# Performance work log

Hardware: AMD Instinct MI355X
Metric: run time of the kernel (lower is better)

## Reference

```python
import jax, jax.numpy as jnp
import numpy as np

WH, WW = 12, 12
NUM_HEADS = 8
NW = 4


def _relative_position_index():
    ch, cw = np.meshgrid(np.arange(WH), np.arange(WW), indexing='ij')
    coords = np.stack([ch, cw]).reshape(2, -1)            # [2, Wh*Ww]
    rel = coords[:, :, None] - coords[:, None, :]         # [2, M, M]
    rel = rel.transpose(1, 2, 0)                          # [M, M, 2]
    rel[:, :, 0] += WH - 1
    rel[:, :, 1] += WW - 1
    rel[:, :, 0] *= 2 * WW - 1
    return jnp.asarray(rel.sum(-1))                       # [M, M] int


def setup_inputs() -> dict:
    key = jax.random.key(0)
    ks = jax.random.split(key, 11)
    C = 512
    B_, N = 512, WH * WW + 1
    std = 0.02
    return {
        'x': jax.random.normal(ks[0], (B_, N, C), dtype=jnp.float32),
        'mask': jnp.zeros((NW, N, N), dtype=jnp.float32),
        'rpb_table': jax.random.normal(ks[1], ((2 * WH - 1) * (2 * WW - 1), NUM_HEADS), dtype=jnp.float32) * std,
        'Wq': jax.random.normal(ks[2], (C, C), dtype=jnp.float32) * (C ** -0.5),
        'bq': jax.random.normal(ks[3], (C,), dtype=jnp.float32) * std,
        'Wk': jax.random.normal(ks[4], (C, C), dtype=jnp.float32) * (C ** -0.5),
        'bk': jax.random.normal(ks[5], (C,), dtype=jnp.float32) * std,
        'Wv': jax.random.normal(ks[6], (C, C), dtype=jnp.float32) * (C ** -0.5),
        'bv': jax.random.normal(ks[7], (C,), dtype=jnp.float32) * std,
        'Wo': jax.random.normal(ks[8], (C, C), dtype=jnp.float32) * (C ** -0.5),
        'bo': jax.random.normal(ks[9], (C,), dtype=jnp.float32) * std,
    }


def reference(x, mask, rpb_table, Wq, bq, Wk, bk, Wv, bv, Wo, bo):
    B_, N, C = x.shape
    H = NUM_HEADS
    hd = C // H
    scale = hd ** -0.5
    B = B_ // NW
    M = WH * WW  # window tokens (N = M + 1 global token)

    def proj(W, b):
        return (x @ W.T + b).reshape(B_, N, H, hd).transpose(0, 2, 1, 3)  # [B_,H,N,hd]

    q = proj(Wq, bq)
    k = proj(Wk, bk)
    v = proj(Wv, bv)

    attn = jnp.einsum('bhnd,bhmd->bhnm', q, k) * scale  # [B_,H,N,N]

    rel_idx = _relative_position_index()                 # [M,M]
    bias = rpb_table[rel_idx].transpose(2, 0, 1)          # [H,M,M]
    attn = attn.at[:, :, :M, :M].add(bias[None])          # N != M: bias on window block only

    # shifted-window mask: (nW, N, N)
    attn = (attn.reshape(B, NW, H, N, N) + mask[None, :, None]).reshape(B_, H, N, N)

    # ---- global-token attention redistribution (gx) ----
    ga = attn[:, :, -1, :].reshape(B, NW, H, N).transpose(0, 2, 1, 3)   # [B,H,NW,N]
    g1 = ga[:, :, :, :M].reshape(B, H, NW * M)                           # window keys, all windows
    g2 = ga[:, :, :, M].mean(-1, keepdims=True)                          # mean global-global logit [B,H,1]
    g = jax.nn.softmax(jnp.concatenate([g1, g2], axis=-1), axis=-1)      # [B,H,NW*M+1]
    g1 = g[:, :, :-1].reshape(B, H, NW, M).transpose(0, 2, 1, 3).reshape(B_, H, M)
    g2 = jnp.broadcast_to(g[:, :, -1][:, None, :], (B, NW, H)).reshape(B_, H, 1)
    ga_full = jnp.concatenate([g1, g2], axis=-1)[:, :, None, :]          # [B_,H,1,N]
    gx = jnp.einsum('bhqn,bhnd->bhqd', ga_full, v).transpose(0, 2, 1, 3).reshape(B_, C)
    gx = gx.reshape(B, NW, C).sum(1)                                     # sum over windows [B,C]
    gx = jnp.broadcast_to(gx[:, None, :], (B, NW, C)).reshape(B_, C)

    # ---- standard window attention ----
    attn = jax.nn.softmax(attn, axis=-1)
    out = jnp.einsum('bhnm,bhmd->bhnd', attn, v).transpose(0, 2, 1, 3).reshape(B_, N, C)
    out = out.at[:, -1, :].set(gx)
    return out @ Wo.T + bo
```

## Files before the change

### kernel.cpp

```cpp
#include <hip/hip_runtime.h>
#include <hip/hip_bf16.h>
#include <stdint.h>

#define NTOK 145
#define MTOK 144
#define CDIM 512
#define NHEAD 8
#define HD 64
#define NWIN 4
#define BWIN 512
#define MROWS (BWIN*NTOK)

typedef short short8 __attribute__((ext_vector_type(8)));
typedef float f32x4 __attribute__((ext_vector_type(4)));

__device__ __forceinline__ uint16_t f2bf(float f) {
  union { float f; uint32_t u; } x; x.f = f;
  uint32_t r = x.u + 0x7FFFu + ((x.u >> 16) & 1u);
  return (uint16_t)(r >> 16);
}
__device__ __forceinline__ float bf2f(uint16_t u) {
  union { uint32_t u; float f; } x; x.u = ((uint32_t)u) << 16; return x.f;
}
__device__ __forceinline__ uint32_t pack2(float a, float b) {
  return (uint32_t)f2bf(a) | ((uint32_t)f2bf(b) << 16);
}

#define GLL(gp, lp) __builtin_amdgcn_global_load_lds( \
    (const __attribute__((address_space(1))) uint32_t*)(gp), \
    (__attribute__((address_space(3))) uint32_t*)(lp), 16, 0, 0)

__global__ __launch_bounds__(256) void cast_x(const float* __restrict__ x,
                                              uint16_t* __restrict__ xb) {
  size_t id = ((size_t)blockIdx.x*256 + threadIdx.x)*8;
  float4 a = *(const float4*)(x+id), c = *(const float4*)(x+id+4);
  uint4 o = make_uint4(pack2(a.x,a.y), pack2(a.z,a.w), pack2(c.x,c.y), pack2(c.z,c.w));
  *(uint4*)(xb+id) = o;
}

__global__ void prep_kernel(const float* __restrict__ rpb,
                            const float* __restrict__ Wq, const float* __restrict__ bq,
                            const float* __restrict__ Wk, const float* __restrict__ bk,
                            const float* __restrict__ Wv, const float* __restrict__ bv,
                            const float* __restrict__ Wo,
                            uint16_t* __restrict__ wqkv, uint16_t* __restrict__ wo,
                            float* __restrict__ bqkv, float* __restrict__ biastab) {
  int id = blockIdx.x * 256 + threadIdx.x;
  const int A = 1536*512, B = 512*512, C2 = 1536, D = 8*144*144;
  if (id < A) {
    int n = id >> 9, k = id & 511;
    const float* W = (n < 512) ? Wq : (n < 1024) ? Wk : Wv;
    wqkv[id] = f2bf(W[(size_t)(n & 511)*512 + k]);
  } else if ((id -= A) < B) {
    wo[id] = f2bf(Wo[id]);
  } else if ((id -= B) < C2) {
    bqkv[id] = (id < 512) ? bq[id] : (id < 1024) ? bk[id-512] : bv[id-1024];
  } else if ((id -= C2) < D) {
    int h = id / (144*144); int rr = id % (144*144);
    int i = rr / 144, j = rr % 144;
    int rel = (i/12 - j/12 + 11) * 23 + (i%12 - j%12 + 11);
    biastab[id] = rpb[rel*8 + h];
  }
}

__global__ __launch_bounds__(256) void gemm_qkv(
    const uint16_t* __restrict__ xb, const uint16_t* __restrict__ wqkv,
    const float* __restrict__ bqkv,
    uint16_t* __restrict__ qb, uint16_t* __restrict__ kb, uint16_t* __restrict__ vb) {
  __shared__ __align__(16) uint16_t As[128*32];
  __shared__ __align__(16) uint16_t Bs[128*32];
  int bid = blockIdx.x;
  int mb, nb;
  if (bid < 6912) { int g = bid / 96, r = bid % 96; mb = g*8 + (r & 7); nb = r >> 3; }
  else           { int r = bid - 6912;              mb = 576 + (r & 3); nb = r >> 2; }
  int tid = threadIdx.x;
  int lane = tid & 63, w = tid >> 6;
  int wm = w >> 1, wn = w & 1;
  int lm = lane & 15, lq = lane >> 4;

  int srow = lane >> 2, scol = (lane & 3) * 8;
  const uint16_t* agp = xb   + (size_t)(mb*128 + w*32 + srow)*512 + scol;
  const uint16_t* bgp = wqkv + (size_t)(nb*128 + w*32 + srow)*512 + scol;
  uint16_t* Asw = &As[w*32*32];
  uint16_t* Bsw = &Bs[w*32*32];

  f32x4 acc[4][4];
#pragma unroll
  for (int a = 0; a < 4; a++)
#pragma unroll
    for (int b = 0; b < 4; b++) acc[a][b] = (f32x4){0.f,0.f,0.f,0.f};

  for (int kt = 0; kt < 16; kt++) {
    GLL(agp + kt*32,          Asw);
    GLL(agp + kt*32 + 16*512, Asw + 16*32);
    GLL(bgp + kt*32,          Bsw);
    GLL(bgp + kt*32 + 16*512, Bsw + 16*32);
    __syncthreads();
    short8 a[4], b[4];
#pragma unroll
    for (int t = 0; t < 4; t++) a[t] = *(short8*)&As[(wm*64 + t*16 + lm)*32 + lq*8];
#pragma unroll
    for (int t = 0; t < 4; t++) b[t] = *(short8*)&Bs[(wn*64 + t*16 + lm)*32 + lq*8];
#pragma unroll
    for (int tm = 0; tm < 4; tm++)
#pragma unroll
      for (int tn = 0; tn < 4; tn++)
        acc[tm][tn] = __builtin_amdgcn_mfma_f32_16x16x32_bf16(a[tm], b[tn], acc[tm][tn], 0, 0, 0);
    __syncthreads();
  }
#pragma unroll
  for (int tn = 0; tn < 4; tn++) {
    int n = nb*128 + wn*64 + tn*16 + lm;
    float bias = bqkv[n];
    int which = n >> 9, c = n & 511;
    uint16_t* dst = (which == 0) ? qb : (which == 1) ? kb : vb;
    int hh = c >> 6, dd = c & 63;
#pragma unroll
    for (int tm = 0; tm < 4; tm++) {
#pragma unroll
      for (int r = 0; r < 4; r++) {
        int m = mb*128 + wm*64 + tm*16 + lq*4 + r;
        int bw = m / 145, nl = m - bw*145;
        dst[((size_t)(bw*8 + hh)*145 + nl)*64 + dd] = f2bf(acc[tm][tn][r] + bias);
      }
    }
  }
}

__global__ __launch_bounds__(256, 2) void attn_kernel(
    const uint16_t* __restrict__ qb, const uint16_t* __restrict__ kb,
    const uint16_t* __restrict__ vb, const float* __restrict__ biastab,
    const float* __restrict__ mask, float* __restrict__ glog,
    uint16_t* __restrict__ attn_out) {
  __shared__ __align__(16) uint16_t P[144*160];
  __shared__ __align__(16) uint16_t vs[145*64];
  int bid = blockIdx.x;
  int b_ = bid >> 3, h = bid & 7;
  int nw = b_ & 3;
  int tid = threadIdx.x, lane = tid & 63, w = tid >> 6;
  int lm = lane & 15, lq = lane >> 4;
  const size_t hbase = ((size_t)(b_*8 + h)) * (145*64);
  const uint16_t* qp = qb + hbase;
  const uint16_t* kp = kb + hbase;
  const uint16_t* vp = vb + hbase;

  for (int c = tid; c < 1160; c += 256)
    *(uint4*)&vs[c*8] = *(const uint4*)(vp + (size_t)c*8);

  int nmt = (w < 2) ? 3 : 2;
  f32x4 acc[3][10];
#pragma unroll
  for (int a = 0; a < 3; a++)
#pragma unroll
    for (int b = 0; b < 10; b++) acc[a][b] = (f32x4){0.f,0.f,0.f,0.f};

#pragma unroll
  for (int ks = 0; ks < 2; ks++) {
    short8 bfr[10];
#pragma unroll
    for (int nt = 0; nt < 10; nt++) {
      int j = nt*16 + lm; if (j > 144) j = 144;
      bfr[nt] = *(const short8*)(kp + (size_t)j*64 + ks*32 + lq*8);
    }
#pragma unroll
    for (int mtl = 0; mtl < 3; mtl++) {
      if (mtl < nmt) {
        int mt = w + mtl*4;
        int i = mt*16 + lm; if (i > 144) i = 144;
        short8 afr = *(const short8*)(qp + (size_t)i*64 + ks*32 + lq*8);
#pragma unroll
        for (int nt = 0; nt < 10; nt++)
          acc[mtl][nt] = __builtin_amdgcn_mfma_f32_16x16x32_bf16(afr, bfr[nt], acc[mtl][nt], 0, 0, 0);
      }
    }
  }

  const float scale = 0.125f;
#pragma unroll
  for (int mtl = 0; mtl < 3; mtl++) {
    if (mtl >= nmt) continue;
    int mt = w + mtl*4;
    if (mt == 9) {
      if (lq == 0) {
#pragma unroll
        for (int nt = 0; nt < 10; nt++) {
          int j = nt*16 + lm;
          if (j < 145)
            glog[(size_t)(b_*8 + h)*145 + j] =
                acc[mtl][nt][0]*scale + mask[(nw*145 + 144)*145 + j];
        }
      }
      continue;
    }
#pragma unroll
    for (int r = 0; r < 4; r++) {
      int i = mt*16 + lq*4 + r;
      float mx = -3.0e38f;
#pragma unroll
      for (int nt = 0; nt < 10; nt++) {
        int j = nt*16 + lm;
        float t = acc[mtl][nt][r]*scale;
        if (j < 145) t += mask[(nw*145 + i)*145 + j];
        if (j < 144) t += biastab[(h*144 + i)*144 + j];
        if (j >= 145) t = -3.0e38f;
        acc[mtl][nt][r] = t;
        mx = fmaxf(mx, t);
      }
#pragma unroll
      for (int off = 1; off < 16; off <<= 1) mx = fmaxf(mx, __shfl_xor(mx, off));
      float sum = 0.f;
#pragma unroll
      for (int nt = 0; nt < 10; nt++) {
        int j = nt*16 + lm;
        float p = (j < 145) ? __expf(acc[mtl][nt][r] - mx) : 0.f;
        acc[mtl][nt][r] = p; sum += p;
      }
#pragma unroll
      for (int off = 1; off < 16; off <<= 1) sum += __shfl_xor(sum, off);
      float rs = __builtin_amdgcn_rcpf(sum);
#pragma unroll
      for (int nt = 0; nt < 10; nt++)
        P[i*160 + nt*16 + lm] = f2bf(acc[mtl][nt][r] * rs);
    }
  }
  __syncthreads();

  f32x4 oacc[9];
#pragma unroll
  for (int a = 0; a < 9; a++) oacc[a] = (f32x4){0.f,0.f,0.f,0.f};
#pragma unroll
  for (int ks = 0; ks < 5; ks++) {
    short8 bfr;
#pragma unroll
    for (int jj = 0; jj < 8; jj++) {
      int j = ks*32 + lq*8 + jj; if (j > 144) j = 144;
      bfr[jj] = (short)vs[j*64 + w*16 + lm];
    }
#pragma unroll
    for (int mt = 0; mt < 9; mt++) {
      short8 afr = *(short8*)&P[(mt*16 + lm)*160 + ks*32 + lq*8];
      oacc[mt] = __builtin_amdgcn_mfma_f32_16x16x32_bf16(afr, bfr, oacc[mt], 0, 0, 0);
    }
  }
#pragma unroll
  for (int mt = 0; mt < 9; mt++) {
#pragma unroll
    for (int r = 0; r < 4; r++) {
      int i = mt*16 + lq*4 + r;
      attn_out[((size_t)b_*145 + i)*512 + h*64 + w*16 + lm] = f2bf(oacc[mt][r]);
    }
  }
}

__global__ __launch_bounds__(256) void gx_kernel(
    const float* __restrict__ glog, const uint16_t* __restrict__ vb,
    uint16_t* __restrict__ attn_out) {
  int bid = blockIdx.x;
  int b = bid >> 3, h = bid & 7;
  int tid = threadIdx.x, lane = tid & 63, w = tid >> 6;
  __shared__ float lg[580];
  __shared__ float pl[576];
  __shared__ float sred[8];
  __shared__ float sacc[256];
  for (int t = tid; t < 580; t += 256) {
    int nwi = t / 145, j = t - nwi*145;
    lg[t] = glog[(size_t)((b*4 + nwi)*8 + h)*145 + j];
  }
  __syncthreads();
  float g2 = 0.25f*(lg[144] + lg[289] + lg[434] + lg[579]);
  float mx = g2;
  for (int t = tid; t < 576; t += 256) {
    int nwi = t / 144, j = t - nwi*144;
    mx = fmaxf(mx, lg[nwi*145 + j]);
  }
#pragma unroll
  for (int off = 1; off < 64; off <<= 1) mx = fmaxf(mx, __shfl_xor(mx, off));
  if (lane == 0) sred[w] = mx;
  __syncthreads();
  mx = fmaxf(fmaxf(sred[0], sred[1]), fmaxf(sred[2], sred[3]));
  float sum = 0.f;
  for (int t = tid; t < 576; t += 256) {
    int nwi = t / 144, j = t - nwi*144;
    float p = __expf(lg[nwi*145 + j] - mx);
    pl[t] = p; sum += p;
  }
#pragma unroll
  for (int off = 1; off < 64; off <<= 1) sum += __shfl_xor(sum, off);
  if (lane == 0) sred[4 + w] = sum;
  __syncthreads();
  sum = (sred[4] + sred[5]) + (sred[6] + sred[7]);
  float p2 = __expf(g2 - mx);
  float rs = __builtin_amdgcn_rcpf(sum + p2);
  const uint16_t* vp = vb + (size_t)((b*4 + w)*8 + h)*(145*64);
  float acc = 0.f;
  int d = lane;
#pragma unroll 4
  for (int j = 0; j < 144; j++)
    acc += pl[w*144 + j] * bf2f(vp[j*64 + d]);
  acc += p2 * bf2f(vp[144*64 + d]);
  sacc[tid] = acc;
  __syncthreads();
  if (w == 0) {
    float tot = (sacc[lane] + sacc[64 + lane]) + (sacc[128 + lane] + sacc[192 + lane]);
    uint16_t o = f2bf(tot * rs);
    for (int nwi = 0; nwi < 4; nwi++)
      attn_out[((size_t)(b*4 + nwi)*145 + 144)*512 + h*64 + d] = o;
  }
}

__global__ __launch_bounds__(256) void gemm_out(
    const uint16_t* __restrict__ A, const uint16_t* __restrict__ wo,
    const float* __restrict__ bo, float* __restrict__ out) {
  __shared__ __align__(16) uint16_t As[128*32];
  __shared__ __align__(16) uint16_t Bs[128*32];
  int bid = blockIdx.x;
  int mb, nb;
  if (bid < 2304) { int g = bid / 32, r = bid % 32; mb = g*8 + (r & 7); nb = r >> 3; }
  else            { int r = bid - 2304;             mb = 576 + (r & 3); nb = r >> 2; }
  int tid = threadIdx.x;
  int lane = tid & 63, w = tid >> 6;
  int wm = w >> 1, wn = w & 1;
  int lm = lane & 15, lq = lane >> 4;

  int srow = lane >> 2, scol = (lane & 3) * 8;
  const uint16_t* agp = A  + (size_t)(mb*128 + w*32 + srow)*512 + scol;
  const uint16_t* bgp = wo + (size_t)(nb*128 + w*32 + srow)*512 + scol;
  uint16_t* Asw = &As[w*32*32];
  uint16_t* Bsw = &Bs[w*32*32];

  f32x4 acc[4][4];
#pragma unroll
  for (int a = 0; a < 4; a++)
#pragma unroll
    for (int b = 0; b < 4; b++) acc[a][b] = (f32x4){0.f,0.f,0.f,0.f};

  for (int kt = 0; kt < 16; kt++) {
    GLL(agp + kt*32,          Asw);
    GLL(agp + kt*32 + 16*512, Asw + 16*32);
    GLL(bgp + kt*32,          Bsw);
    GLL(bgp + kt*32 + 16*512, Bsw + 16*32);
    __syncthreads();
    short8 a[4], b[4];
#pragma unroll
    for (int t = 0; t < 4; t++) a[t] = *(short8*)&As[(wm*64 + t*16 + lm)*32 + lq*8];
#pragma unroll
    for (int t = 0; t < 4; t++) b[t] = *(short8*)&Bs[(wn*64 + t*16 + lm)*32 + lq*8];
#pragma unroll
    for (int tm = 0; tm < 4; tm++)
#pragma unroll
      for (int tn = 0; tn < 4; tn++)
        acc[tm][tn] = __builtin_amdgcn_mfma_f32_16x16x32_bf16(a[tm], b[tn], acc[tm][tn], 0, 0, 0);
    __syncthreads();
  }
#pragma unroll
  for (int tn = 0; tn < 4; tn++) {
    int n = nb*128 + wn*64 + tn*16 + lm;
    float bias = bo[n];
#pragma unroll
    for (int tm = 0; tm < 4; tm++) {
#pragma unroll
      for (int r = 0; r < 4; r++) {
        int m = mb*128 + wm*64 + tm*16 + lq*4 + r;
        out[(size_t)m*512 + n] = acc[tm][tn][r] + bias;
      }
    }
  }
}

extern "C" void kernel_launch(void* const* d_in, const int* in_sizes, int n_in,
                              void* d_out, int out_size, void* d_ws, size_t ws_size,
                              hipStream_t stream) {
  const float* x    = (const float*)d_in[0];
  const float* mask = (const float*)d_in[1];
  const float* rpb  = (const float*)d_in[2];
  const float* Wq   = (const float*)d_in[3];
  const float* bq   = (const float*)d_in[4];
  const float* Wk   = (const float*)d_in[5];
  const float* bk   = (const float*)d_in[6];
  const float* Wv   = (const float*)d_in[7];
  const float* bv   = (const float*)d_in[8];
  const float* Wo   = (const float*)d_in[9];
  const float* bo   = (const float*)d_in[10];

  uint8_t* ws = (uint8_t*)d_ws;
  size_t off = 0;
  auto alloc = [&](size_t bytes) -> void* {
    void* p = ws + off; off += (bytes + 255) & ~(size_t)255; return p;
  };
  uint16_t* wqkv   = (uint16_t*)alloc((size_t)1536*512*2);
  uint16_t* wo     = (uint16_t*)alloc((size_t)512*512*2);
  float*    bqkv   = (float*)alloc(1536*4);
  float*    biastab= (float*)alloc((size_t)8*144*144*4);
  float*    glog   = (float*)alloc((size_t)512*8*145*4);
  uint16_t* xb     = (uint16_t*)alloc((size_t)MROWS*512*2);
  uint16_t* qb     = (uint16_t*)alloc((size_t)MROWS*512*2);
  uint16_t* kb     = (uint16_t*)alloc((size_t)MROWS*512*2);
  uint16_t* vb     = (uint16_t*)alloc((size_t)MROWS*512*2);
  uint16_t* attn   = (uint16_t*)alloc((size_t)MROWS*512*2);

  cast_x<<<18560, 256, 0, stream>>>(x, xb);
  prep_kernel<<<4750, 256, 0, stream>>>(rpb, Wq, bq, Wk, bk, Wv, bv, Wo,
                                        wqkv, wo, bqkv, biastab);
  gemm_qkv<<<580*12, 256, 0, stream>>>(xb, wqkv, bqkv, qb, kb, vb);
  attn_kernel<<<4096, 256, 0, stream>>>(qb, kb, vb, biastab, mask, glog, attn);
  gx_kernel<<<1024, 256, 0, stream>>>(glog, vb, attn);
  gemm_out<<<580*4, 256, 0, stream>>>(attn, wo, bo, (float*)d_out);
}
```

Before: 726.1 us.

## Merge mask and position bias into bf16 table, restructure attention per-warp with transposed V

Precomputes a combined bf16 mask+relative-position-bias table per (window, head) in the prep kernel, so the attention kernel reads one bf16 value per score instead of two fp32 tables. The attention kernel is reorganized so each warp processes one query tile at a time end to end (QK, softmax, PV) using a private P buffer. V is stored transposed in LDS for vectorized B-fragment loads. This cuts register and LDS use so occupancy can go to 3 blocks per CU. The risks are bf16 rounding of the bias/mask and the cost of the strided transposed LDS writes.

New measurement: 784.2 us. 1.08x slower.

```diff
diff --git a/kernel.cpp b/kernel.cpp
--- a/kernel.cpp
+++ b/kernel.cpp
@@ -39,14 +39,15 @@
 }
 
 __global__ void prep_kernel(const float* __restrict__ rpb,
+                            const float* __restrict__ mask,
                             const float* __restrict__ Wq, const float* __restrict__ bq,
                             const float* __restrict__ Wk, const float* __restrict__ bk,
                             const float* __restrict__ Wv, const float* __restrict__ bv,
                             const float* __restrict__ Wo,
                             uint16_t* __restrict__ wqkv, uint16_t* __restrict__ wo,
-                            float* __restrict__ bqkv, float* __restrict__ biastab) {
+                            float* __restrict__ bqkv, uint16_t* __restrict__ mbias) {
   int id = blockIdx.x * 256 + threadIdx.x;
-  const int A = 1536*512, B = 512*512, C2 = 1536, D = 8*144*144;
+  const int A = 1536*512, B = 512*512, C2 = 1536, D = 32*145*145;
   if (id < A) {
     int n = id >> 9, k = id & 511;
     const float* W = (n < 512) ? Wq : (n < 1024) ? Wk : Wv;
@@ -56,10 +57,15 @@
   } else if ((id -= B) < C2) {
     bqkv[id] = (id < 512) ? bq[id] : (id < 1024) ? bk[id-512] : bv[id-1024];
   } else if ((id -= C2) < D) {
-    int h = id / (144*144); int rr = id % (144*144);
-    int i = rr / 144, j = rr % 144;
-    int rel = (i/12 - j/12 + 11) * 23 + (i%12 - j%12 + 11);
-    biastab[id] = rpb[rel*8 + h];
+    int s = id / (145*145); int rr = id % (145*145);
+    int i = rr / 145, j = rr % 145;
+    int nw = s >> 3, h = s & 7;
+    float v = mask[(nw*145 + i)*145 + j];
+    if (i < 144 && j < 144) {
+      int rel = (i/12 - j/12 + 11) * 23 + (i%12 - j%12 + 11);
+      v += rpb[rel*8 + h];
+    }
+    mbias[id] = f2bf(v);
   }
 }
 
@@ -127,13 +133,12 @@
   }
 }
 
-__global__ __launch_bounds__(256, 2) void attn_kernel(
+__global__ __launch_bounds__(256, 3) void attn_kernel(
     const uint16_t* __restrict__ qb, const uint16_t* __restrict__ kb,
-    const uint16_t* __restrict__ vb, const float* __restrict__ biastab,
-    const float* __restrict__ mask, float* __restrict__ glog,
-    uint16_t* __restrict__ attn_out) {
-  __shared__ __align__(16) uint16_t P[144*160];
-  __shared__ __align__(16) uint16_t vs[145*64];
+    const uint16_t* __restrict__ vb, const uint16_t* __restrict__ mbias,
+    float* __restrict__ glog, uint16_t* __restrict__ attn_out) {
+  __shared__ __align__(16) uint16_t vt[64*168];
+  __shared__ __align__(16) uint16_t Pw[4][16*168];
   int bid = blockIdx.x;
   int b_ = bid >> 3, h = bid & 7;
   int nw = b_ & 3;
@@ -143,67 +148,66 @@
   const uint16_t* qp = qb + hbase;
   const uint16_t* kp = kb + hbase;
   const uint16_t* vp = vb + hbase;
-
-  for (int c = tid; c < 1160; c += 256)
-    *(uint4*)&vs[c*8] = *(const uint4*)(vp + (size_t)c*8);
+  const uint16_t* mb = mbias + (size_t)(nw*8 + h)*(145*145);
+
+  for (int c = tid; c < 1160; c += 256) {
+    int j = c >> 3, d0 = (c & 7) * 8;
+    uint4 u = *(const uint4*)(vp + (size_t)j*64 + d0);
+    const uint16_t* e = (const uint16_t*)&u;
+#pragma unroll
+    for (int t = 0; t < 8; t++) vt[(d0 + t)*168 + j] = e[t];
+  }
+  for (int t = tid; t < 64*23; t += 256) {
+    int d = t / 23, j = 145 + t % 23;
+    vt[d*168 + j] = 0;
+  }
+  __syncthreads();
+
+  const float scale = 0.125f;
+  uint16_t* myP = Pw[w];
 
   int nmt = (w < 2) ? 3 : 2;
-  f32x4 acc[3][10];
-#pragma unroll
-  for (int a = 0; a < 3; a++)
-#pragma unroll
-    for (int b = 0; b < 10; b++) acc[a][b] = (f32x4){0.f,0.f,0.f,0.f};
-
-#pragma unroll
-  for (int ks = 0; ks < 2; ks++) {
-    short8 bfr[10];
-#pragma unroll
-    for (int nt = 0; nt < 10; nt++) {
-      int j = nt*16 + lm; if (j > 144) j = 144;
-      bfr[nt] = *(const short8*)(kp + (size_t)j*64 + ks*32 + lq*8);
-    }
-#pragma unroll
-    for (int mtl = 0; mtl < 3; mtl++) {
-      if (mtl < nmt) {
-        int mt = w + mtl*4;
-        int i = mt*16 + lm; if (i > 144) i = 144;
-        short8 afr = *(const short8*)(qp + (size_t)i*64 + ks*32 + lq*8);
-#pragma unroll
-        for (int nt = 0; nt < 10; nt++)
-          acc[mtl][nt] = __builtin_amdgcn_mfma_f32_16x16x32_bf16(afr, bfr[nt], acc[mtl][nt], 0, 0, 0);
-      }
-    }
-  }
-
-  const float scale = 0.125f;
-#pragma unroll
-  for (int mtl = 0; mtl < 3; mtl++) {
-    if (mtl >= nmt) continue;
+  for (int mtl = 0; mtl < nmt; mtl++) {
     int mt = w + mtl*4;
+    f32x4 acc[10];
+#pragma unroll
+    for (int nt = 0; nt < 10; nt++) acc[nt] = (f32x4){0.f,0.f,0.f,0.f};
+#pragma unroll
+    for (int ks = 0; ks < 2; ks++) {
+      int i = mt*16 + lm; if (i > 144) i = 144;
+      short8 afr = *(const short8*)(qp + (size_t)i*64 + ks*32 + lq*8);
+#pragma unroll
+      for (int nt = 0; nt < 10; nt++) {
+        int j = nt*16 + lm; if (j > 144) j = 144;
+        short8 bfr = *(const short8*)(kp + (size_t)j*64 + ks*32 + lq*8);
+        acc[nt] = __builtin_amdgcn_mfma_f32_16x16x32_bf16(afr, bfr, acc[nt], 0, 0, 0);
+      }
+    }
+
     if (mt == 9) {
       if (lq == 0) {
 #pragma unroll
         for (int nt = 0; nt < 10; nt++) {
           int j = nt*16 + lm;
           if (j < 145)
-            glog[(size_t)(b_*8 + h)*145 + j] =
-                acc[mtl][nt][0]*scale + mask[(nw*145 + 144)*145 + j];
+            glog[(size_t)(b_*8 + h)*145 + j] = acc[nt][0]*scale + bf2f(mb[144*145 + j]);
         }
       }
       continue;
     }
+
 #pragma unroll
     for (int r = 0; r < 4; r++) {
       int i = mt*16 + lq*4 + r;
+      const uint16_t* mrow = mb + i*145;
       float mx = -3.0e38f;
 #pragma unroll
       for (int nt = 0; nt < 10; nt++) {
         int j = nt*16 + lm;
-        float t = acc[mtl][nt][r]*scale;
-        if (j < 145) t += mask[(nw*145 + i)*145 + j];
-        if (j < 144) t += biastab[(h*144 + i)*144 + j];
+        int jc = (j > 144) ? 144 : j;
+        float t = acc[nt][r]*scale + bf2f(mrow[jc]);
         if (j >= 145) t = -3.0e38f;
-        acc[mtl][nt][r] = t;
+        acc[nt][r] = t;
         mx = fmaxf(mx, t);
       }
 #pragma unroll
@@ -212,42 +216,37 @@
 #pragma unroll
       for (int nt = 0; nt < 10; nt++) {
         int j = nt*16 + lm;
-        float p = (j < 145) ? __expf(acc[mtl][nt][r] - mx) : 0.f;
-        acc[mtl][nt][r] = p; sum += p;
+        float p = (j < 145) ? __expf(acc[nt][r] - mx) : 0.f;
+        acc[nt][r] = p; sum += p;
       }
 #pragma unroll
       for (int off = 1; off < 16; off <<= 1) sum += __shfl_xor(sum, off);
       float rs = __builtin_amdgcn_rcpf(sum);
+      int ri = lq*4 + r;
 #pragma unroll
       for (int nt = 0; nt < 10; nt++)
-        P[i*160 + nt*16 + lm] = f2bf(acc[mtl][nt][r] * rs);
-    }
-  }
-  __syncthreads();
-
-  f32x4 oacc[9];
-#pragma unroll
-  for (int a = 0; a < 9; a++) oacc[a] = (f32x4){0.f,0.f,0.f,0.f};
-#pragma unroll
-  for (int ks = 0; ks < 5; ks++) {
-    short8 bfr;
-#pragma unroll
-    for (int jj = 0; jj < 8; jj++) {
-      int j = ks*32 + lq*8 + jj; if (j > 144) j = 144;
-      bfr[jj] = (short)vs[j*64 + w*16 + lm];
-    }
-#pragma unroll
-    for (int mt = 0; mt < 9; mt++) {
-      short8 afr = *(short8*)&P[(mt*16 + lm)*160 + ks*32 + lq*8];
-      oacc[mt] = __builtin_amdgcn_mfma_f32_16x16x32_bf16(afr, bfr, oacc[mt], 0, 0, 0);
-    }
-  }
-#pragma unroll
-  for (int mt = 0; mt < 9; mt++) {
-#pragma unroll
-    for (int r = 0; r < 4; r++) {
-      int i = mt*16 + lq*4 + r;
-      attn_out[((size_t)b_*145 + i)*512 + h*64 + w*16 + lm] = f2bf(oacc[mt][r]);
+        myP[ri*168 + nt*16 + lm] = f2bf(acc[nt][r] * rs);
+    }
+
+    f32x4 oacc[4];
+#pragma unroll
+    for (int dt = 0; dt < 4; dt++) oacc[dt] = (f32x4){0.f,0.f,0.f,0.f};
+#pragma unroll
+    for (int ks = 0; ks < 5; ks++) {
+      short8 afr = *(short8*)&myP[lm*168 + ks*32 + lq*8];
+#pragma unroll
+      for (int dt = 0; dt < 4; dt++) {
+        short8 bfr = *(short8*)&vt[(dt*16 + lm)*168 + ks*32 + lq*8];
+        oacc[dt] = __builtin_amdgcn_mfma_f32_16x16x32_bf16(afr, bfr, oacc[dt], 0, 0, 0);
+      }
+    }
+#pragma unroll
+    for (int dt = 0; dt < 4; dt++) {
+#pragma unroll
+      for (int r = 0; r < 4; r++) {
+        int i = mt*16 + lq*4 + r;
+        attn_out[((size_t)b_*145 + i)*512 + h*64 + dt*16 + lm] = f2bf(oacc[dt][r]);
+      }
     }
   }
 }
@@ -390,7 +389,7 @@
   uint16_t* wqkv   = (uint16_t*)alloc((size_t)1536*512*2);
   uint16_t* wo     = (uint16_t*)alloc((size_t)512*512*2);
   float*    bqkv   = (float*)alloc(1536*4);
-  float*    biastab= (float*)alloc((size_t)8*144*144*4);
+  uint16_t* mbias  = (uint16_t*)alloc((size_t)32*145*145*2);
   float*    glog   = (float*)alloc((size_t)512*8*145*4);
   uint16_t* xb     = (uint16_t*)alloc((size_t)MROWS*512*2);
   uint16_t* qb     = (uint16_t*)alloc((size_t)MROWS*512*2);
@@ -399,10 +398,10 @@
   uint16_t* attn   = (uint16_t*)alloc((size_t)MROWS*512*2);
 
   cast_x<<<18560, 256, 0, stream>>>(x, xb);
-  prep_kernel<<<4750, 256, 0, stream>>>(rpb, Wq, bq, Wk, bk, Wv, bv, Wo,
-                                        wqkv, wo, bqkv, biastab);
+  prep_kernel<<<6731, 256, 0, stream>>>(rpb, mask, Wq, bq, Wk, bk, Wv, bv, Wo,
+                                        wqkv, wo, bqkv, mbias);
   gemm_qkv<<<580*12, 256, 0, stream>>>(xb, wqkv, bqkv, qb, kb, vb);
-  attn_kernel<<<4096, 256, 0, stream>>>(qb, kb, vb, biastab, mask, glog, attn);
+  attn_kernel<<<4096, 256, 0, stream>>>(qb, kb, vb, mbias, glog, attn);
   gx_kernel<<<1024, 256, 0, stream>>>(glog, vb, attn);
   gemm_out<<<580*4, 256, 0, stream>>>(attn, wo, bo, (float*)d_out);
 }
```
